# Performance work log

Hardware: AMD Instinct MI355X
Metric: run time of the kernel (lower is better)

Reference implementation:

```python
import jax, jax.numpy as jnp
import numpy as np

EMBED = 2048
T = 2048  # max_seq_length
BATCH = 2  # hardcoded by the module's initial-state shape


def setup_inputs() -> dict:
    key = jax.random.key(0)
    ks = jax.random.split(key, 7)
    s = 0.02
    return {
        "x": jax.random.normal(ks[0], (BATCH, EMBED), dtype=jnp.float32),
        "W_ih": jax.random.normal(ks[1], (4 * EMBED, EMBED), dtype=jnp.float32) * s,
        "W_hh": jax.random.normal(ks[2], (4 * EMBED, EMBED), dtype=jnp.float32) * s,
        "b_ih": jax.random.normal(ks[3], (4 * EMBED,), dtype=jnp.float32) * s,
        "b_hh": jax.random.normal(ks[4], (4 * EMBED,), dtype=jnp.float32) * s,
        "W_out": jax.random.normal(ks[5], (EMBED, EMBED), dtype=jnp.float32) * s,
        "b_out": jax.random.normal(ks[6], (EMBED,), dtype=jnp.float32) * s,
    }


def reference(x, W_ih, W_hh, b_ih, b_hh, W_out, b_out):
    E = x.shape[-1]

    def step(carry, _):
        inp, h, c = carry  # each [B, E]
        gates = inp @ W_ih.T + b_ih + h @ W_hh.T + b_hh  # [B, 4E]
        i, f, g, o = jnp.split(gates, 4, axis=-1)  # PyTorch gate order i,f,g,o
        c_new = jax.nn.sigmoid(f) * c + jax.nn.sigmoid(i) * jnp.tanh(g)
        h_new = jax.nn.sigmoid(o) * jnp.tanh(c_new)
        # output of single-layer LSTM == h_new; it is fed back as next input
        return (h_new, h_new, c_new), h_new

    h0 = jnp.zeros((x.shape[0], E), dtype=x.dtype)
    c0 = jnp.zeros((x.shape[0], E), dtype=x.dtype)
    _, seq = jax.lax.scan(step, (x, h0, c0), None, length=T)  # [T, B, E]

    out = seq @ W_out.T + b_out  # dropout is identity in eval
    return jnp.transpose(out, (1, 0, 2))  # [B, T, E]
```

## Files before the change

### kernel.cpp

```cpp
#include <hip/hip_runtime.h>
#include <hip/hip_fp16.h>
#include <stdint.h>


#define E 2048
#define NBLK 256
#define NTHR 512
#define HLDS_B 2304
#define PLS_STRIDE 20
#define PLS_PAR 640
#define SMEM_MAIN 23680
#define SMEM_PROJ 131072

typedef uint32_t u32;
typedef unsigned long long u64;

__device__ __forceinline__ float sigf(float x){
  return __builtin_amdgcn_rcpf(1.0f + __expf(-x));
}
__device__ __forceinline__ float tanhfast(float x){
  float e = __expf(2.0f * x);
  return 1.0f - 2.0f * __builtin_amdgcn_rcpf(e + 1.0f);
}

#define ROWFMA8(W0, W1, W2, W3, A0, A1) \
  A0 = fmaf(__low2float(W0),  p0.x, A0); A0 = fmaf(__high2float(W0), p0.y, A0); \
  A0 = fmaf(__low2float(W1),  p0.z, A0); A0 = fmaf(__high2float(W1), p0.w, A0); \
  A0 = fmaf(__low2float(W2),  p1.x, A0); A0 = fmaf(__high2float(W2), p1.y, A0); \
  A0 = fmaf(__low2float(W3),  p1.z, A0); A0 = fmaf(__high2float(W3), p1.w, A0); \
  A1 = fmaf(__low2float(W0),  q0.x, A1); A1 = fmaf(__high2float(W0), q0.y, A1); \
  A1 = fmaf(__low2float(W1),  q0.z, A1); A1 = fmaf(__high2float(W1), q0.w, A1); \
  A1 = fmaf(__low2float(W2),  q1.x, A1); A1 = fmaf(__high2float(W2), q1.y, A1); \
  A1 = fmaf(__low2float(W3),  q1.z, A1); A1 = fmaf(__high2float(W3), q1.w, A1);

#define POLLCHK(J, UJ) \
  if (pend & (1 << J)){ \
    if ((u32)(UJ >> 32) == tag){ \
      hlds[cdst[J]] = __uint_as_float((u32)UJ); \
      pend &= ~(1 << J); \
    } \
  }

#define ISSUE8(R0, R1, R2, R3, R4, R5, R6, R7) \
  asm volatile( \
    "global_load_dwordx2 %0, %8, off sc0 sc1\n\t" \
    "global_load_dwordx2 %1, %8, off offset:512 sc0 sc1\n\t" \
    "global_load_dwordx2 %2, %8, off offset:1024 sc0 sc1\n\t" \
    "global_load_dwordx2 %3, %8, off offset:1536 sc0 sc1\n\t" \
    "global_load_dwordx2 %4, %8, off offset:2048 sc0 sc1\n\t" \
    "global_load_dwordx2 %5, %8, off offset:2560 sc0 sc1\n\t" \
    "global_load_dwordx2 %6, %8, off offset:3072 sc0 sc1\n\t" \
    "global_load_dwordx2 %7, %8, off offset:3584 sc0 sc1" \
    : "=&v"(R0), "=&v"(R1), "=&v"(R2), "=&v"(R3), \
      "=&v"(R4), "=&v"(R5), "=&v"(R6), "=&v"(R7) \
    : "v"(src) : "memory")

#define RELOAD(J, UJ, OFS) \
  if (pend & (1 << J)){ \
    asm volatile("global_load_dwordx2 %0, %1, off offset:" OFS " sc0 sc1" \
                 : "=v"(UJ) : "v"(src) : "memory"); \
  }

__global__ void __launch_bounds__(NTHR, 1) lstm_kernel(
    const float* __restrict__ xin, const float* __restrict__ Wih,
    const float* __restrict__ Whh, const float* __restrict__ bih,
    const float* __restrict__ bhh, u64* __restrict__ chk,
    float* __restrict__ seqout)
{
  extern __shared__ char smem[];
  float* hlds = (float*)smem;
  float* pls  = (float*)(smem + 18432);
  float* bias = (float*)(smem + 23552);

  const int tid  = threadIdx.x;
  const int blk  = blockIdx.x;
  const int e0   = blk << 3;
  const int lane = tid & 63;
  const int wv   = tid >> 6;
  const int rg   = lane >> 3;
  const int ksl  = lane & 7;
  const int ks   = (wv << 3) + ksl;
  const int k0   = ks << 5;

  if (tid < 32){
    const int grow = ((tid >> 3) << 11) + e0 + (tid & 7);
    bias[tid] = bih[grow] + bhh[grow];
  }
  for (int i = tid; i < 2 * E; i += NTHR){
    const int b = i >> 11, k = i & 2047;
    hlds[b * HLDS_B + (k >> 5) * 36 + (k & 31)] = xin[i];
  }
  __syncthreads();

  const float* hb0 = hlds + ks * 36;
  const float* hb1 = hlds + HLDS_B + ks * 36;

  __half2 wh[64];
  float acc0[4] = {0.f, 0.f, 0.f, 0.f};
  float acc1[4] = {0.f, 0.f, 0.f, 0.f};
  #pragma unroll
  for (int rr = 0; rr < 4; ++rr){
    const int row  = (rg << 2) + rr;
    const int grow = ((row >> 3) << 11) + e0 + (row & 7);
    const float* pa = Wih + (size_t)grow * E + k0;
    const float* pb = Whh + (size_t)grow * E + k0;
    #pragma unroll
    for (int c = 0; c < 8; ++c){
      float4 a = *(const float4*)(pa + (c << 2));
      float4 b = *(const float4*)(pb + (c << 2));
      wh[(rr << 4) + (c << 1)    ] =
        __halves2half2(__float2half_rn(a.x + b.x), __float2half_rn(a.y + b.y));
      wh[(rr << 4) + (c << 1) + 1] =
        __halves2half2(__float2half_rn(a.z + b.z), __float2half_rn(a.w + b.w));
      float4 x0 = *(const float4*)(hb0 + (c << 2));
      float4 x1 = *(const float4*)(hb1 + (c << 2));
      acc0[rr] = fmaf(a.x, x0.x, acc0[rr]); acc0[rr] = fmaf(a.y, x0.y, acc0[rr]);
      acc0[rr] = fmaf(a.z, x0.z, acc0[rr]); acc0[rr] = fmaf(a.w, x0.w, acc0[rr]);
      acc1[rr] = fmaf(a.x, x1.x, acc1[rr]); acc1[rr] = fmaf(a.y, x1.y, acc1[rr]);
      acc1[rr] = fmaf(a.z, x1.z, acc1[rr]); acc1[rr] = fmaf(a.w, x1.w, acc1[rr]);
    }
  }

  const float br = bias[lane & 31];
  float creg = 0.0f;

  int cdst[8];
  #pragma unroll
  for (int j = 0; j < 8; ++j){
    const int c = (wv << 9) + (j << 6) + lane;
    const int b = (c >> 3) & 1;
    const int e = ((c >> 4) << 3) | (c & 7);
    cdst[j] = b * HLDS_B + (e >> 5) * 36 + (e & 31);
  }
  u64* const pchk0 = chk;
  u64* const pchk1 = chk + 4096;

  for (int t = 0; t < 2048; ++t){
    #pragma unroll
    for (int m = 1; m <= 4; m <<= 1){
      #pragma unroll
      for (int rr = 0; rr < 4; ++rr){
        acc0[rr] += __shfl_xor(acc0[rr], m, 64);
        acc1[rr] += __shfl_xor(acc1[rr], m, 64);
      }
    }
    if (ksl == 0){
      float2* pw = (float2*)(pls + (t & 1) * PLS_PAR);
      #pragma unroll
      for (int rr = 0; rr < 4; ++rr)
        pw[((rg << 2) + rr) * (PLS_STRIDE / 2) + wv] = make_float2(acc0[rr], acc1[rr]);
    }
    __syncthreads();

    if (wv == 0){
      const int r = lane & 31;
      const int b = lane >> 5;
      const float* rp = pls + (t & 1) * PLS_PAR + r * PLS_STRIDE;
      float4 v0 = *(const float4*)(rp);
      float4 v1 = *(const float4*)(rp + 4);
      float4 v2 = *(const float4*)(rp + 8);
      float4 v3 = *(const float4*)(rp + 12);
      float s = br + (b ? (v0.y + v0.w + v1.y + v1.w + v2.y + v2.w + v3.y + v3.w)
                        : (v0.x + v0.z + v1.x + v1.z + v2.x + v2.z + v3.x + v3.z));
      const float gi = s;
      const float gf = __shfl(s, (lane + 8)  & 63, 64);
      const float gg = __shfl(s, (lane + 16) & 63, 64);
      const float go = __shfl(s, (lane + 24) & 63, 64);
      if (r < 8){
        const float cn = sigf(gf) * creg + sigf(gi) * tanhfast(gg);
        const float hn = sigf(go) * tanhfast(cn);
        creg = cn;
        if (t < 2047){
          const u64 pk = ((u64)(u32)(t + 1) << 32) | (u64)__float_as_uint(hn);
          u64* dst = (((t + 1) & 1) ? pchk1 : pchk0) + (blk << 4) + (b << 3) + r;
          asm volatile("global_store_dwordx2 %0, %1, off sc0 sc1"
                       :: "v"(dst), "v"(pk) : "memory");
        }
        seqout[(((size_t)b << 11) + (size_t)t) * E + e0 + r] = hn;
      }
    }
    if (t == 2047) break;

    {
      const u64* src = (((t + 1) & 1) ? pchk1 : pchk0) + (wv << 9) + lane;
      const u32 tag = (u32)(t + 1);
      u64 a0_, a1_, a2_, a3_, a4_, a5_, a6_, a7_;
      ISSUE8(a0_, a1_, a2_, a3_, a4_, a5_, a6_, a7_);
      asm volatile("s_waitcnt vmcnt(0)" ::: "memory");
      int pend = 0xFF;
      while (true){
        POLLCHK(0, a0_) POLLCHK(1, a1_) POLLCHK(2, a2_) POLLCHK(3, a3_)
        POLLCHK(4, a4_) POLLCHK(5, a5_) POLLCHK(6, a6_) POLLCHK(7, a7_)
        if (pend == 0) break;
        __builtin_amdgcn_s_sleep(1);
        RELOAD(0, a0_, "0")    RELOAD(1, a1_, "512")
        RELOAD(2, a2_, "1024") RELOAD(3, a3_, "1536")
        RELOAD(4, a4_, "2048") RELOAD(5, a5_, "2560")
        RELOAD(6, a6_, "3072") RELOAD(7, a7_, "3584")
        asm volatile("s_waitcnt vmcnt(0)" ::: "memory");
      }
      asm volatile("s_waitcnt lgkmcnt(0)" ::: "memory");
      __builtin_amdgcn_sched_barrier(0);
    }

    #pragma unroll
    for (int rr = 0; rr < 4; ++rr){ acc0[rr] = 0.f; acc1[rr] = 0.f; }
    #pragma unroll
    for (int c8 = 0; c8 < 4; ++c8){
      float4 p0 = *(const float4*)(hb0 + (c8 << 3));
      float4 p1 = *(const float4*)(hb0 + (c8 << 3) + 4);
      float4 q0 = *(const float4*)(hb1 + (c8 << 3));
      float4 q1 = *(const float4*)(hb1 + (c8 << 3) + 4);
      #pragma unroll
      for (int rr = 0; rr < 4; ++rr){
        ROWFMA8(wh[(rr << 4) + (c8 << 2)],     wh[(rr << 4) + (c8 << 2) + 1],
                wh[(rr << 4) + (c8 << 2) + 2], wh[(rr << 4) + (c8 << 2) + 3],
                acc0[rr], acc1[rr]);
      }
    }
  }
}

__global__ void __launch_bounds__(256, 1) proj_kernel(
    float* __restrict__ io, const float* __restrict__ Wout,
    const float* __restrict__ bout)
{
  extern __shared__ char smem[];
  float* alds = (float*)smem;
  const int tid = threadIdx.x;
  const size_t rbase = (size_t)blockIdx.x * 16 * E;

  for (int idx = tid; idx < 8192; idx += 256){
    float4 v = *(const float4*)(io + rbase + ((size_t)idx << 2));
    *(float4*)(alds + (idx << 2)) = v;
  }
  __syncthreads();

  for (int p = 0; p < 2; ++p){
    const int n0 = (p << 10) + tid;
    const int n1 = n0 + 256;
    const int n2 = n0 + 512;
    const int n3 = n0 + 768;
    const float* wr0 = Wout + (size_t)n0 * E;
    const float* wr1 = Wout + (size_t)n1 * E;
    const float* wr2 = Wout + (size_t)n2 * E;
    const float* wr3 = Wout + (size_t)n3 * E;
    float acc0[16], acc1[16], acc2[16], acc3[16];
    #pragma unroll
    for (int m = 0; m < 16; ++m){
      acc0[m] = 0.0f; acc1[m] = 0.0f; acc2[m] = 0.0f; acc3[m] = 0.0f;
    }
    for (int kc = 0; kc < 256; ++kc){
      const float4 a0v = *(const float4*)(wr0 + (kc << 3));
      const float4 a1v = *(const float4*)(wr0 + (kc << 3) + 4);
      const float4 b0v = *(const float4*)(wr1 + (kc << 3));
      const float4 b1v = *(const float4*)(wr1 + (kc << 3) + 4);
      const float4 c0v = *(const float4*)(wr2 + (kc << 3));
      const float4 c1v = *(const float4*)(wr2 + (kc << 3) + 4);
      const float4 d0v = *(const float4*)(wr3 + (kc << 3));
      const float4 d1v = *(const float4*)(wr3 + (kc << 3) + 4);
      const float* ap = alds + (kc << 3);
      #pragma unroll
      for (int m = 0; m < 16; ++m){
        const float* a = ap + (m << 11);
        float4 x0 = *(const float4*)(a);
        float4 x1 = *(const float4*)(a + 4);
        acc0[m] = fmaf(a0v.x, x0.x, acc0[m]); acc0[m] = fmaf(a0v.y, x0.y, acc0[m]);
        acc0[m] = fmaf(a0v.z, x0.z, acc0[m]); acc0[m] = fmaf(a0v.w, x0.w, acc0[m]);
        acc0[m] = fmaf(a1v.x, x1.x, acc0[m]); acc0[m] = fmaf(a1v.y, x1.y, acc0[m]);
        acc0[m] = fmaf(a1v.z, x1.z, acc0[m]); acc0[m] = fmaf(a1v.w, x1.w, acc0[m]);
        acc1[m] = fmaf(b0v.x, x0.x, acc1[m]); acc1[m] = fmaf(b0v.y, x0.y, acc1[m]);
        acc1[m] = fmaf(b0v.z, x0.z, acc1[m]); acc1[m] = fmaf(b0v.w, x0.w, acc1[m]);
        acc1[m] = fmaf(b1v.x, x1.x, acc1[m]); acc1[m] = fmaf(b1v.y, x1.y, acc1[m]);
        acc1[m] = fmaf(b1v.z, x1.z, acc1[m]); acc1[m] = fmaf(b1v.w, x1.w, acc1[m]);
        acc2[m] = fmaf(c0v.x, x0.x, acc2[m]); acc2[m] = fmaf(c0v.y, x0.y, acc2[m]);
        acc2[m] = fmaf(c0v.z, x0.z, acc2[m]); acc2[m] = fmaf(c0v.w, x0.w, acc2[m]);
        acc2[m] = fmaf(c1v.x, x1.x, acc2[m]); acc2[m] = fmaf(c1v.y, x1.y, acc2[m]);
        acc2[m] = fmaf(c1v.z, x1.z, acc2[m]); acc2[m] = fmaf(c1v.w, x1.w, acc2[m]);
        acc3[m] = fmaf(d0v.x, x0.x, acc3[m]); acc3[m] = fmaf(d0v.y, x0.y, acc3[m]);
        acc3[m] = fmaf(d0v.z, x0.z, acc3[m]); acc3[m] = fmaf(d0v.w, x0.w, acc3[m]);
        acc3[m] = fmaf(d1v.x, x1.x, acc3[m]); acc3[m] = fmaf(d1v.y, x1.y, acc3[m]);
        acc3[m] = fmaf(d1v.z, x1.z, acc3[m]); acc3[m] = fmaf(d1v.w, x1.w, acc3[m]);
      }
    }
    const float bo0 = bout[n0];
    const float bo1 = bout[n1];
    const float bo2 = bout[n2];
    const float bo3 = bout[n3];
    #pragma unroll
    for (int m = 0; m < 16; ++m){
      io[rbase + ((size_t)m << 11) + n0] = acc0[m] + bo0;
      io[rbase + ((size_t)m << 11) + n1] = acc1[m] + bo1;
      io[rbase + ((size_t)m << 11) + n2] = acc2[m] + bo2;
      io[rbase + ((size_t)m << 11) + n3] = acc3[m] + bo3;
    }
  }
}

extern "C" void kernel_launch(void* const* d_in, const int* in_sizes, int n_in,
                              void* d_out, int out_size, void* d_ws, size_t ws_size,
                              hipStream_t stream)
{
  const float* xin  = (const float*)d_in[0];
  const float* Wih  = (const float*)d_in[1];
  const float* Whh  = (const float*)d_in[2];
  const float* bih  = (const float*)d_in[3];
  const float* bhh  = (const float*)d_in[4];
  const float* Wout = (const float*)d_in[5];
  const float* bout = (const float*)d_in[6];
  float* out = (float*)d_out;

  u64* chk = (u64*)d_ws;

  hipFuncSetAttribute((const void*)lstm_kernel,
                      hipFuncAttributeMaxDynamicSharedMemorySize, SMEM_MAIN);
  hipFuncSetAttribute((const void*)proj_kernel,
                      hipFuncAttributeMaxDynamicSharedMemorySize, SMEM_PROJ);

  void* args[] = { (void*)&xin, (void*)&Wih, (void*)&Whh, (void*)&bih, (void*)&bhh,
                   (void*)&chk, (void*)&out };
  hipLaunchCooperativeKernel((const void*)lstm_kernel, dim3(NBLK), dim3(NTHR),
                             args, SMEM_MAIN, stream);

  proj_kernel<<<256, 256, SMEM_PROJ, stream>>>(out, Wout, bout);
}
```

Baseline: 8.163 ms.

## Copy hidden sequence to workspace and project with paired 32-row fp16 tiles

The output projection now first copies the LSTM hidden-state sequence into workspace. A new kernel then has each block load 32 rows of it into shared memory as packed fp16 and compute 1024 output columns with 4x32 register accumulators, halving the number of Wout reads per row. The copy is needed because outputs are written in place over rows that a sibling block still reads. It adds a full extra pass over 32 MB and rounds the activations to fp16, at some cost in precision. The sleep in the polling loop is also moved to after the reload loads are issued.

```diff
diff --git a/kernel.cpp b/kernel.cpp
--- a/kernel.cpp
+++ b/kernel.cpp
@@ -192,11 +192,11 @@
         POLLCHK(0, a0_) POLLCHK(1, a1_) POLLCHK(2, a2_) POLLCHK(3, a3_)
         POLLCHK(4, a4_) POLLCHK(5, a5_) POLLCHK(6, a6_) POLLCHK(7, a7_)
         if (pend == 0) break;
-        __builtin_amdgcn_s_sleep(1);
         RELOAD(0, a0_, "0")    RELOAD(1, a1_, "512")
         RELOAD(2, a2_, "1024") RELOAD(3, a3_, "1536")
         RELOAD(4, a4_, "2048") RELOAD(5, a5_, "2560")
         RELOAD(6, a6_, "3072") RELOAD(7, a7_, "3584")
+        __builtin_amdgcn_s_sleep(1);
         asm volatile("s_waitcnt vmcnt(0)" ::: "memory");
       }
       asm volatile("s_waitcnt lgkmcnt(0)" ::: "memory");
@@ -218,6 +218,95 @@
                 acc0[rr], acc1[rr]);
       }
     }
+  }
+}
+
+__global__ void copy_kernel(const float* __restrict__ s, float* __restrict__ d)
+{
+  const size_t i = (((size_t)blockIdx.x << 8) + threadIdx.x) << 2;
+  *(float4*)(d + i) = *(const float4*)(s + i);
+}
+
+__global__ void __launch_bounds__(256, 1) proj_pair_kernel(
+    const float* __restrict__ src, float* __restrict__ io,
+    const float* __restrict__ Wout, const float* __restrict__ bout)
+{
+  extern __shared__ char smem[];
+  u32* ah = (u32*)smem;
+  const int tid = threadIdx.x;
+  const int blk = blockIdx.x;
+  const size_t rbase = (size_t)(blk >> 1) * 32 * E;
+  const int ch = (blk & 1) << 10;
+
+  for (int idx = tid; idx < 32768; idx += 256){
+    const float2 v = *(const float2*)(src + rbase + ((size_t)idx << 1));
+    ah[idx] = (u32)__half_as_ushort(__float2half_rn(v.x))
+            | ((u32)__half_as_ushort(__float2half_rn(v.y)) << 16);
+  }
+  __syncthreads();
+
+  const int n0 = ch + tid;
+  const int n1 = n0 + 256;
+  const int n2 = n0 + 512;
+  const int n3 = n0 + 768;
+  const float* wr0 = Wout + (size_t)n0 * E;
+  const float* wr1 = Wout + (size_t)n1 * E;
+  const float* wr2 = Wout + (size_t)n2 * E;
+  const float* wr3 = Wout + (size_t)n3 * E;
+  float acc0[32], acc1[32], acc2[32], acc3[32];
+  #pragma unroll
+  for (int m = 0; m < 32; ++m){
+    acc0[m] = 0.0f; acc1[m] = 0.0f; acc2[m] = 0.0f; acc3[m] = 0.0f;
+  }
+  for (int kc = 0; kc < 256; ++kc){
+    const float4 a0v = *(const float4*)(wr0 + (kc << 3));
+    const float4 a1v = *(const float4*)(wr0 + (kc << 3) + 4);
+    const float4 b0v = *(const float4*)(wr1 + (kc << 3));
+    const float4 b1v = *(const float4*)(wr1 + (kc << 3) + 4);
+    const float4 c0v = *(const float4*)(wr2 + (kc << 3));
+    const float4 c1v = *(const float4*)(wr2 + (kc << 3) + 4);
+    const float4 d0v = *(const float4*)(wr3 + (kc << 3));
+    const float4 d1v = *(const float4*)(wr3 + (kc << 3) + 4);
+    const u32* hp = ah + (kc << 2);
+    #pragma unroll
+    for (int m = 0; m < 32; ++m){
+      const uint4 hv = *(const uint4*)(hp + (m << 10));
+      const __half2 h0 = __builtin_bit_cast(__half2, hv.x);
+      const __half2 h1 = __builtin_bit_cast(__half2, hv.y);
+      const __half2 h2 = __builtin_bit_cast(__half2, hv.z);
+      const __half2 h3 = __builtin_bit_cast(__half2, hv.w);
+      const float x0 = __low2float(h0), x1 = __high2float(h0);
+      const float x2 = __low2float(h1), x3 = __high2float(h1);
+      const float x4 = __low2float(h2), x5 = __high2float(h2);
+      const float x6 = __low2float(h3), x7 = __high2float(h3);
+      acc0[m] = fmaf(a0v.x, x0, acc0[m]); acc0[m] = fmaf(a0v.y, x1, acc0[m]);
+      acc0[m] = fmaf(a0v.z, x2, acc0[m]); acc0[m] = fmaf(a0v.w, x3, acc0[m]);
+      acc0[m] = fmaf(a1v.x, x4, acc0[m]); acc0[m] = fmaf(a1v.y, x5, acc0[m]);
+      acc0[m] = fmaf(a1v.z, x6, acc0[m]); acc0[m] = fmaf(a1v.w, x7, acc0[m]);
+      acc1[m] = fmaf(b0v.x, x0, acc1[m]); acc1[m] = fmaf(b0v.y, x1, acc1[m]);
+      acc1[m] = fmaf(b0v.z, x2, acc1[m]); acc1[m] = fmaf(b0v.w, x3, acc1[m]);
+      acc1[m] = fmaf(b1v.x, x4, acc1[m]); acc1[m] = fmaf(b1v.y, x5, acc1[m]);
+      acc1[m] = fmaf(b1v.z, x6, acc1[m]); acc1[m] = fmaf(b1v.w, x7, acc1[m]);
+      acc2[m] = fmaf(c0v.x, x0, acc2[m]); acc2[m] = fmaf(c0v.y, x1, acc2[m]);
+      acc2[m] = fmaf(c0v.z, x2, acc2[m]); acc2[m] = fmaf(c0v.w, x3, acc2[m]);
+      acc2[m] = fmaf(c1v.x, x4, acc2[m]); acc2[m] = fmaf(c1v.y, x5, acc2[m]);
+      acc2[m] = fmaf(c1v.z, x6, acc2[m]); acc2[m] = fmaf(c1v.w, x7, acc2[m]);
+      acc3[m] = fmaf(d0v.x, x0, acc3[m]); acc3[m] = fmaf(d0v.y, x1, acc3[m]);
+      acc3[m] = fmaf(d0v.z, x2, acc3[m]); acc3[m] = fmaf(d0v.w, x3, acc3[m]);
+      acc3[m] = fmaf(d1v.x, x4, acc3[m]); acc3[m] = fmaf(d1v.y, x5, acc3[m]);
+      acc3[m] = fmaf(d1v.z, x6, acc3[m]); acc3[m] = fmaf(d1v.w, x7, acc3[m]);
+    }
+  }
+  const float bo0 = bout[n0];
+  const float bo1 = bout[n1];
+  const float bo2 = bout[n2];
+  const float bo3 = bout[n3];
+  #pragma unroll
+  for (int m = 0; m < 32; ++m){
+    io[rbase + ((size_t)m << 11) + n0] = acc0[m] + bo0;
+    io[rbase + ((size_t)m << 11) + n1] = acc1[m] + bo1;
+    io[rbase + ((size_t)m << 11) + n2] = acc2[m] + bo2;
+    io[rbase + ((size_t)m << 11) + n3] = acc3[m] + bo3;
   }
 }
 
@@ -311,9 +400,12 @@
   float* out = (float*)d_out;
 
   u64* chk = (u64*)d_ws;
+  const size_t SEQ_BYTES = (size_t)2 * 2048 * E * sizeof(float);
 
   hipFuncSetAttribute((const void*)lstm_kernel,
                       hipFuncAttributeMaxDynamicSharedMemorySize, SMEM_MAIN);
+  hipFuncSetAttribute((const void*)proj_pair_kernel,
+                      hipFuncAttributeMaxDynamicSharedMemorySize, SMEM_PROJ);
   hipFuncSetAttribute((const void*)proj_kernel,
                       hipFuncAttributeMaxDynamicSharedMemorySize, SMEM_PROJ);
 
@@ -322,5 +414,11 @@
   hipLaunchCooperativeKernel((const void*)lstm_kernel, dim3(NBLK), dim3(NTHR),
                              args, SMEM_MAIN, stream);
 
-  proj_kernel<<<256, 256, SMEM_PROJ, stream>>>(out, Wout, bout);
-}
+  if (ws_size >= 65536 + SEQ_BYTES){
+    float* scp = (float*)((char*)d_ws + 65536);
+    copy_kernel<<<8192, 256, 0, stream>>>(out, scp);
+    proj_pair_kernel<<<256, 256, SMEM_PROJ, stream>>>(scp, out, Wout, bout);
+  } else {
+    proj_kernel<<<256, 256, SMEM_PROJ, stream>>>(out, Wout, bout);
+  }
+}
```

Measured after the change: 8.081 ms. Within noise of the previous version (-1.0%).
